# Kernel tuning notes

Measured on AMD Instinct MI355X. Metric: run time of the kernel, lower is better.

Reference implementation:

```python
import jax, jax.numpy as jnp
import numpy as np

N = 8192
INPUT_DIM = 512
R = 2
HID = INPUT_DIM // R  # 256
OUTPUT_DIM = 512


def _linear_params(key, out_dim, in_dim):
    kw, kb = jax.random.split(key)
    bound = 1.0 / np.sqrt(in_dim)
    w = jax.random.uniform(kw, (out_dim, in_dim), jnp.float32, -bound, bound)
    b = jax.random.uniform(kb, (out_dim,), jnp.float32, -bound, bound)
    return w, b


def setup_inputs() -> dict:
    key = jax.random.key(0)
    k0, k1, k2, k3, k4 = jax.random.split(key, 5)
    O0 = jax.random.normal(k0, (N, INPUT_DIM), dtype=jnp.float32)
    W_w, W_b = _linear_params(k1, HID, INPUT_DIM)
    U_w, U_b = _linear_params(k2, HID, INPUT_DIM)
    H_w, H_b = _linear_params(k3, HID, INPUT_DIM)
    fc0_w, fc0_b = _linear_params(k4, OUTPUT_DIM, HID)
    return {"O0": O0, "W_w": W_w, "W_b": W_b, "U_w": U_w, "U_b": U_b,
            "H_w": H_w, "H_b": H_b, "fc0_w": fc0_w, "fc0_b": fc0_b}


def reference(O0, W_w, W_b, U_w, U_b, H_w, H_b, fc0_w, fc0_b):
    q = O0 @ W_w.T + W_b          # [N, HID]
    k = O0 @ U_w.T + U_b          # [N, HID]
    v = O0 @ H_w.T + H_b          # [N, HID]
    # NOTE: no 1/sqrt(d) scaling, faithful to the original module.
    scores = q @ k.T              # [N, N]
    R1 = jax.nn.softmax(scores, axis=1)
    O1 = (R1 @ v) @ fc0_w.T + fc0_b  # [N, OUTPUT_DIM]
    return O1
```

## Files before the change

kernel.cpp:

```cpp
#include <hip/hip_runtime.h>

#define N_TOK 8192
#define IN_DIM 512
#define HID 256
#define OUT_DIM 512

typedef _Float16 v8h __attribute__((ext_vector_type(8)));
typedef float v4f __attribute__((ext_vector_type(4)));

__device__ inline void async_copy16(const void* g, void* l) {
    __builtin_amdgcn_global_load_lds(
        (const __attribute__((address_space(1))) void*)g,
        (__attribute__((address_space(3))) void*)l, 16, 0, 0);
}

__global__ __launch_bounds__(256)
void conv_f16(const float* __restrict__ in, _Float16* __restrict__ out) {
    const size_t i = ((size_t)blockIdx.x * 256 + threadIdx.x) * 8;
    float4 f0 = *(const float4*)&in[i];
    float4 f1 = *(const float4*)&in[i + 4];
    union { _Float16 h[8]; uint4 u; } pk;
    pk.h[0] = (_Float16)f0.x; pk.h[1] = (_Float16)f0.y;
    pk.h[2] = (_Float16)f0.z; pk.h[3] = (_Float16)f0.w;
    pk.h[4] = (_Float16)f1.x; pk.h[5] = (_Float16)f1.y;
    pk.h[6] = (_Float16)f1.z; pk.h[7] = (_Float16)f1.w;
    *(uint4*)&out[i] = pk.u;
}

__global__ __launch_bounds__(256)
void proj_qkv(const _Float16* __restrict__ O0h,
              const float* __restrict__ W_w, const float* __restrict__ W_b,
              const float* __restrict__ U_w, const float* __restrict__ U_b,
              const float* __restrict__ H_w, const float* __restrict__ H_b,
              _Float16* __restrict__ qb, _Float16* __restrict__ kb,
              _Float16* __restrict__ vt) {
    __shared__ _Float16 As[128][72];
    __shared__ _Float16 Bs[64][72];

    const int t = threadIdx.x;
    const int wv = t >> 6;
    const int lane = t & 63;
    const int quad = lane >> 4;
    const int lm = lane & 15;
    const int m0 = blockIdx.x * 128;
    const int n0 = blockIdx.y * 64;
    const int z = blockIdx.z;

    const float* B    = (z == 0) ? W_w : (z == 1) ? U_w : H_w;
    const float* bias = (z == 0) ? W_b : (z == 1) ? U_b : H_b;

    v4f acc[2][4];
#pragma unroll
    for (int rs = 0; rs < 2; rs++)
#pragma unroll
        for (int ct = 0; ct < 4; ct++) acc[rs][ct] = (v4f){0.f, 0.f, 0.f, 0.f};

    for (int k0 = 0; k0 < IN_DIM; k0 += 64) {
        __syncthreads();
#pragma unroll
        for (int i = 0; i < 4; i++) {
            int slot = t + 256 * i;
            int ar = slot >> 3, ac8 = slot & 7;
            *(uint4*)&As[ar][ac8 * 8] =
                *(const uint4*)&O0h[(size_t)(m0 + ar) * IN_DIM + k0 + ac8 * 8];
        }
#pragma unroll
        for (int i = 0; i < 4; i++) {
            int slot = t + 256 * i;
            int br = slot >> 4, bc4 = slot & 15;
            float4 f = *(const float4*)&B[(size_t)(n0 + br) * IN_DIM + k0 + bc4 * 4];
            union { _Float16 h[4]; uint2 u; } pk;
            pk.h[0] = (_Float16)f.x; pk.h[1] = (_Float16)f.y;
            pk.h[2] = (_Float16)f.z; pk.h[3] = (_Float16)f.w;
            *(uint2*)&Bs[br][bc4 * 4] = pk.u;
        }
        __syncthreads();

#pragma unroll
        for (int kc = 0; kc < 2; kc++) {
            v8h a0 = *(const v8h*)&As[wv * 32 + lm][kc * 32 + quad * 8];
            v8h a1 = *(const v8h*)&As[wv * 32 + 16 + lm][kc * 32 + quad * 8];
            v8h b[4];
#pragma unroll
            for (int ct = 0; ct < 4; ct++)
                b[ct] = *(const v8h*)&Bs[ct * 16 + lm][kc * 32 + quad * 8];
#pragma unroll
            for (int ct = 0; ct < 4; ct++) {
                acc[0][ct] = __builtin_amdgcn_mfma_f32_16x16x32_f16(a0, b[ct], acc[0][ct], 0, 0, 0);
                acc[1][ct] = __builtin_amdgcn_mfma_f32_16x16x32_f16(a1, b[ct], acc[1][ct], 0, 0, 0);
            }
        }
    }

    if (z < 2) {
        _Float16* outp = (z == 0) ? qb : kb;
#pragma unroll
        for (int rs = 0; rs < 2; rs++)
#pragma unroll
            for (int ct = 0; ct < 4; ct++) {
                const int col = n0 + ct * 16 + lm;
                const float bv = bias[col];
#pragma unroll
                for (int r = 0; r < 4; r++) {
                    const int row = m0 + wv * 32 + rs * 16 + quad * 4 + r;
                    outp[(size_t)row * HID + col] = (_Float16)(acc[rs][ct][r] + bv);
                }
            }
    } else {
#pragma unroll
        for (int rs = 0; rs < 2; rs++)
#pragma unroll
            for (int ct = 0; ct < 4; ct++) {
                const int col = n0 + ct * 16 + lm;
                const float bv = bias[col];
                const int rowbase = m0 + wv * 32 + rs * 16 + quad * 4;
                union { _Float16 h[4]; uint2 u; } pk;
#pragma unroll
                for (int r = 0; r < 4; r++) pk.h[r] = (_Float16)(acc[rs][ct][r] + bv);
                *(uint2*)&vt[(size_t)col * N_TOK + rowbase] = pk.u;
            }
    }
}

__global__ __launch_bounds__(256, 2)
void flash_mfma(const _Float16* __restrict__ qb, const _Float16* __restrict__ kb,
                const _Float16* __restrict__ vt,
                _Float16* __restrict__ partA,
                _Float16* __restrict__ partB,
                float* __restrict__ mbuf, float* __restrict__ lbuf,
                int keys_per_part) {
    __shared__ _Float16 Ks[32][256];
    __shared__ _Float16 Vs[2][256][32];

    const int t = threadIdx.x;
    const int w = t >> 6;
    const int lane = t & 63;
    const int quad = lane >> 4;
    const int lm = lane & 15;
    const int p = blockIdx.x & 7;
    const int m0 = (blockIdx.x >> 3) * 128 + w * 32;

    _Float16* part = (p < 4) ? partA + (size_t)p * N_TOK * HID
                             : partB + (size_t)(p - 4) * N_TOK * HID;

    v8h aq[2][8];
#pragma unroll
    for (int rs = 0; rs < 2; rs++)
#pragma unroll
        for (int c = 0; c < 8; c++)
            aq[rs][c] = *(const v8h*)&qb[(size_t)(m0 + rs * 16 + lm) * HID + c * 32 + quad * 8];

    v4f o[2][16];
    float mr[2], lr[2];
#pragma unroll
    for (int rs = 0; rs < 2; rs++) {
#pragma unroll
        for (int dt = 0; dt < 16; dt++) o[rs][dt] = (v4f){0.f, 0.f, 0.f, 0.f};
        mr[rs] = -1e30f; lr[rs] = 0.f;
    }

    const int n_start = p * keys_per_part;
    const int iters = keys_per_part / 32;

    auto issue_K = [&](int n0) {
#pragma unroll
        for (int i = 0; i < 4; i++) {
            int slot = t + 256 * i;
            int kr = slot >> 5, cpos = slot & 31;
            int kc = (cpos - kr) & 31;
            int m = kr & 15;
            int src = ((m >> 2) << 3) + ((kr >> 4) << 2) + (m & 3);
            async_copy16(&kb[(size_t)(n0 + src) * HID + kc * 8],
                         (_Float16*)Ks + (size_t)slot * 8);
        }
    };
    auto issue_V = [&](int n0, int b) {
#pragma unroll
        for (int i = 0; i < 4; i++) {
            int slot = t + 256 * i;
            int d = slot >> 2, c = slot & 3;
            async_copy16(&vt[(size_t)d * N_TOK + n0 + c * 8],
                         (_Float16*)Vs[b] + (size_t)slot * 8);
        }
    };

    issue_V(n_start, 0);
    issue_K(n_start);

    for (int it = 0; it < iters; it++) {
        __syncthreads();

        v4f s[2][2];
#pragma unroll
        for (int rs = 0; rs < 2; rs++)
#pragma unroll
            for (int nt = 0; nt < 2; nt++) s[rs][nt] = (v4f){0.f, 0.f, 0.f, 0.f};
#pragma unroll
        for (int c = 0; c < 8; c++) {
            const int kc = c * 4 + quad;
            const int cp0 = (kc + lm) & 31;
            const int cp1 = (kc + 16 + lm) & 31;
            v8h b0 = *(const v8h*)((const _Float16*)Ks + lm * 256 + cp0 * 8);
            v8h b1 = *(const v8h*)((const _Float16*)Ks + (16 + lm) * 256 + cp1 * 8);
            s[0][0] = __builtin_amdgcn_mfma_f32_16x16x32_f16(b0, aq[0][c], s[0][0], 0, 0, 0);
            s[0][1] = __builtin_amdgcn_mfma_f32_16x16x32_f16(b1, aq[0][c], s[0][1], 0, 0, 0);
            s[1][0] = __builtin_amdgcn_mfma_f32_16x16x32_f16(b0, aq[1][c], s[1][0], 0, 0, 0);
            s[1][1] = __builtin_amdgcn_mfma_f32_16x16x32_f16(b1, aq[1][c], s[1][1], 0, 0, 0);
        }

        __syncthreads();
        if (it + 1 < iters) {
            issue_K(n_start + (it + 1) * 32);
            issue_V(n_start + (it + 1) * 32, (it + 1) & 1);
        }

        v8h bp[2];
#pragma unroll
        for (int rs = 0; rs < 2; rs++) {
            float tm = s[rs][0][0];
#pragma unroll
            for (int r = 1; r < 4; r++) tm = fmaxf(tm, s[rs][0][r]);
#pragma unroll
            for (int r = 0; r < 4; r++) tm = fmaxf(tm, s[rs][1][r]);
            tm = fmaxf(tm, __shfl_xor(tm, 16));
            tm = fmaxf(tm, __shfl_xor(tm, 32));
            float mn = fmaxf(mr[rs], tm);
            if (__any((int)(mn > mr[rs]))) {
                float al = __expf(mr[rs] - mn);
                lr[rs] *= al;
#pragma unroll
                for (int dt = 0; dt < 16; dt++)
#pragma unroll
                    for (int r = 0; r < 4; r++) o[rs][dt][r] *= al;
            }
            mr[rs] = mn;
            float ls = 0.f;
            v8h bpv;
#pragma unroll
            for (int j = 0; j < 4; j++) {
                float p0 = __expf(s[rs][0][j] - mn);
                float p1 = __expf(s[rs][1][j] - mn);
                bpv[j] = (_Float16)p0;
                bpv[j + 4] = (_Float16)p1;
                ls += p0 + p1;
            }
            ls += __shfl_xor(ls, 16);
            ls += __shfl_xor(ls, 32);
            lr[rs] += ls;
            bp[rs] = bpv;
        }

        const _Float16* VsB = (const _Float16*)Vs[it & 1];
#pragma unroll
        for (int dt = 0; dt < 16; dt++) {
            v8h av = *(const v8h*)(VsB + (dt * 16 + lm) * 32 + quad * 8);
            o[0][dt] = __builtin_amdgcn_mfma_f32_16x16x32_f16(av, bp[0], o[0][dt], 0, 0, 0);
            o[1][dt] = __builtin_amdgcn_mfma_f32_16x16x32_f16(av, bp[1], o[1][dt], 0, 0, 0);
        }
    }

#pragma unroll
    for (int rs = 0; rs < 2; rs++) {
        const float inv = 1.0f / lr[rs];
        const int row = m0 + rs * 16 + lm;
#pragma unroll
        for (int dt = 0; dt < 16; dt++) {
            union { _Float16 h[4]; uint2 u; } pk;
#pragma unroll
            for (int r = 0; r < 4; r++) pk.h[r] = (_Float16)(o[rs][dt][r] * inv);
            *(uint2*)&part[(size_t)row * HID + dt * 16 + quad * 4] = pk.u;
        }
        if (quad == 0) {
            mbuf[p * N_TOK + row] = mr[rs];
            lbuf[p * N_TOK + row] = lr[rs];
        }
    }
}

__global__ __launch_bounds__(256)
void combine_parts(_Float16* __restrict__ attn,
                   const _Float16* __restrict__ partA, const _Float16* __restrict__ partB,
                   const float* __restrict__ mbuf, const float* __restrict__ lbuf,
                   int P) {
    const int gid = blockIdx.x * 256 + threadIdx.x;
    const int row = gid >> 5;
    const int c8 = (gid & 31) * 8;

    float M = -1e30f;
    for (int p = 0; p < P; p++) M = fmaxf(M, mbuf[p * N_TOK + row]);
    float den = 0.f;
    float acc[8];
#pragma unroll
    for (int j = 0; j < 8; j++) acc[j] = 0.f;
    for (int p = 0; p < P; p++) {
        float wgt = lbuf[p * N_TOK + row] * __expf(mbuf[p * N_TOK + row] - M);
        den += wgt;
        const _Float16* base = (p < 4) ? partA + (size_t)p * N_TOK * HID
                                       : partB + (size_t)(p - 4) * N_TOK * HID;
        v8h y = *(const v8h*)&base[(size_t)row * HID + c8];
#pragma unroll
        for (int j = 0; j < 8; j++) acc[j] += wgt * (float)y[j];
    }
    const float inv = 1.0f / den;
    union { _Float16 h[8]; uint4 u; } pk;
#pragma unroll
    for (int j = 0; j < 8; j++) pk.h[j] = (_Float16)(acc[j] * inv);
    *(uint4*)&attn[(size_t)row * HID + c8] = pk.u;
}

__global__ __launch_bounds__(256)
void mfma_fc0(const _Float16* __restrict__ Ah, const float* __restrict__ B,
              const float* __restrict__ bias, float* __restrict__ Cout,
              int K, int NC) {
    __shared__ _Float16 As[128][72];
    __shared__ _Float16 Bs[64][72];

    const int t = threadIdx.x;
    const int wv = t >> 6;
    const int lane = t & 63;
    const int quad = lane >> 4;
    const int lm = lane & 15;
    const int m0 = blockIdx.x * 128;
    const int n0 = blockIdx.y * 64;

    v4f acc[2][4];
#pragma unroll
    for (int rs = 0; rs < 2; rs++)
#pragma unroll
        for (int ct = 0; ct < 4; ct++) acc[rs][ct] = (v4f){0.f, 0.f, 0.f, 0.f};

    for (int k0 = 0; k0 < K; k0 += 64) {
        __syncthreads();
#pragma unroll
        for (int i = 0; i < 4; i++) {
            int slot = t + 256 * i;
            int ar = slot >> 3, ac8 = slot & 7;
            *(uint4*)&As[ar][ac8 * 8] =
                *(const uint4*)&Ah[(size_t)(m0 + ar) * K + k0 + ac8 * 8];
        }
#pragma unroll
        for (int i = 0; i < 4; i++) {
            int slot = t + 256 * i;
            int br = slot >> 4, bc4 = slot & 15;
            float4 f = *(const float4*)&B[(size_t)(n0 + br) * K + k0 + bc4 * 4];
            union { _Float16 h[4]; uint2 u; } pk;
            pk.h[0] = (_Float16)f.x; pk.h[1] = (_Float16)f.y;
            pk.h[2] = (_Float16)f.z; pk.h[3] = (_Float16)f.w;
            *(uint2*)&Bs[br][bc4 * 4] = pk.u;
        }
        __syncthreads();

#pragma unroll
        for (int kc = 0; kc < 2; kc++) {
            v8h a0 = *(const v8h*)&As[wv * 32 + lm][kc * 32 + quad * 8];
            v8h a1 = *(const v8h*)&As[wv * 32 + 16 + lm][kc * 32 + quad * 8];
            v8h b[4];
#pragma unroll
            for (int ct = 0; ct < 4; ct++)
                b[ct] = *(const v8h*)&Bs[ct * 16 + lm][kc * 32 + quad * 8];
#pragma unroll
            for (int ct = 0; ct < 4; ct++) {
                acc[0][ct] = __builtin_amdgcn_mfma_f32_16x16x32_f16(a0, b[ct], acc[0][ct], 0, 0, 0);
                acc[1][ct] = __builtin_amdgcn_mfma_f32_16x16x32_f16(a1, b[ct], acc[1][ct], 0, 0, 0);
            }
        }
    }

#pragma unroll
    for (int rs = 0; rs < 2; rs++)
#pragma unroll
        for (int ct = 0; ct < 4; ct++) {
            const int col = n0 + ct * 16 + lm;
            const float bv = bias[col];
#pragma unroll
            for (int r = 0; r < 4; r++) {
                const int row = m0 + wv * 32 + rs * 16 + quad * 4 + r;
                Cout[(size_t)row * NC + col] = acc[rs][ct][r] + bv;
            }
        }
}

extern "C" void kernel_launch(void* const* d_in, const int* in_sizes, int n_in,
                              void* d_out, int out_size, void* d_ws, size_t ws_size,
                              hipStream_t stream) {
    const float* O0    = (const float*)d_in[0];
    const float* W_w   = (const float*)d_in[1];
    const float* W_b   = (const float*)d_in[2];
    const float* U_w   = (const float*)d_in[3];
    const float* U_b   = (const float*)d_in[4];
    const float* H_w   = (const float*)d_in[5];
    const float* H_b   = (const float*)d_in[6];
    const float* fc0_w = (const float*)d_in[7];
    const float* fc0_b = (const float*)d_in[8];

    char* ws = (char*)d_ws;
    _Float16* qb    = (_Float16*)ws;
    _Float16* kb    = (_Float16*)(ws + ((size_t)4 << 20));
    _Float16* vt    = (_Float16*)(ws + ((size_t)8 << 20));
    float*    mbuf  = (float*)(ws + ((size_t)12 << 20));
    float*    lbuf  = mbuf + 8 * N_TOK;
    _Float16* partB = (_Float16*)(ws + ((size_t)16 << 20));
    _Float16* attn  = qb;
    _Float16* O0h   = (_Float16*)d_out;
    _Float16* partA = (_Float16*)d_out;

    const int P = 8;
    const int kpp = N_TOK / P;

    dim3 blk(256);
    conv_f16<<<dim3(N_TOK * IN_DIM / 8 / 256), blk, 0, stream>>>(O0, O0h);

    proj_qkv<<<dim3(N_TOK / 128, HID / 64, 3), blk, 0, stream>>>(
        O0h, W_w, W_b, U_w, U_b, H_w, H_b, qb, kb, vt);

    flash_mfma<<<dim3((N_TOK / 128) * P), blk, 0, stream>>>(
        qb, kb, vt, partA, partB, mbuf, lbuf, kpp);

    combine_parts<<<dim3(N_TOK * HID / 8 / 256), blk, 0, stream>>>(
        attn, partA, partB, mbuf, lbuf, P);

    mfma_fc0<<<dim3(N_TOK / 128, OUT_DIM / 64), blk, 0, stream>>>(
        attn, fc0_w, fc0_b, (float*)d_out, HID, OUT_DIM);
}
```

Baseline: 218.3 us.

## Pre-convert weights, double-buffer GEMM loads, use 512-thread flash blocks

All weight matrices are converted to fp16 in one combined conversion kernel with O0, so the projection and fc0 GEMMs no longer convert fp32 weights inside their tile loops. Those GEMMs now use async global-to-LDS copies into a double-buffered, XOR-swizzled shared layout that overlaps the next tile's load with MFMA work. The flash attention kernel moves to 512 threads, each wave owning 16 query rows instead of 32, to cut register pressure and raise occupancy. In exchange, each K/V tile is reused by fewer MFMAs per wave.

After: 234.7 us. 7.5% more time.

```diff
diff --git a/kernel.cpp b/kernel.cpp
--- a/kernel.cpp
+++ b/kernel.cpp
@@ -15,27 +15,42 @@
 }
 
 __global__ __launch_bounds__(256)
-void conv_f16(const float* __restrict__ in, _Float16* __restrict__ out) {
-    const size_t i = ((size_t)blockIdx.x * 256 + threadIdx.x) * 8;
-    float4 f0 = *(const float4*)&in[i];
-    float4 f1 = *(const float4*)&in[i + 4];
+void conv_all(const float* __restrict__ O0, const float* __restrict__ W_w,
+              const float* __restrict__ U_w, const float* __restrict__ H_w,
+              const float* __restrict__ fc0_w,
+              _Float16* __restrict__ O0h, _Float16* __restrict__ Wh,
+              _Float16* __restrict__ Uh, _Float16* __restrict__ Hh,
+              _Float16* __restrict__ fh) {
+    const int b = blockIdx.x;
+    const float* src; _Float16* dst; size_t off;
+    if (b < 2048) { src = O0; dst = O0h; off = (size_t)b * 2048; }
+    else {
+        int wsel = (b - 2048) >> 6, wb = (b - 2048) & 63;
+        src = (wsel == 0) ? W_w : (wsel == 1) ? U_w : (wsel == 2) ? H_w : fc0_w;
+        dst = (wsel == 0) ? Wh  : (wsel == 1) ? Uh  : (wsel == 2) ? Hh  : fh;
+        off = (size_t)wb * 2048;
+    }
+    const size_t i = off + (size_t)threadIdx.x * 8;
+    float4 f0 = *(const float4*)&src[i];
+    float4 f1 = *(const float4*)&src[i + 4];
     union { _Float16 h[8]; uint4 u; } pk;
     pk.h[0] = (_Float16)f0.x; pk.h[1] = (_Float16)f0.y;
     pk.h[2] = (_Float16)f0.z; pk.h[3] = (_Float16)f0.w;
     pk.h[4] = (_Float16)f1.x; pk.h[5] = (_Float16)f1.y;
     pk.h[6] = (_Float16)f1.z; pk.h[7] = (_Float16)f1.w;
-    *(uint4*)&out[i] = pk.u;
+    *(uint4*)&dst[i] = pk.u;
 }
 
 __global__ __launch_bounds__(256)
 void proj_qkv(const _Float16* __restrict__ O0h,
-              const float* __restrict__ W_w, const float* __restrict__ W_b,
-              const float* __restrict__ U_w, const float* __restrict__ U_b,
-              const float* __restrict__ H_w, const float* __restrict__ H_b,
+              const _Float16* __restrict__ Wh, const _Float16* __restrict__ Uh,
+              const _Float16* __restrict__ Hh,
+              const float* __restrict__ W_b, const float* __restrict__ U_b,
+              const float* __restrict__ H_b,
               _Float16* __restrict__ qb, _Float16* __restrict__ kb,
               _Float16* __restrict__ vt) {
-    __shared__ _Float16 As[128][72];
-    __shared__ _Float16 Bs[64][72];
+    __shared__ _Float16 As[2][128 * 64];
+    __shared__ _Float16 Bs[2][64 * 64];
 
     const int t = threadIdx.x;
     const int wv = t >> 6;
@@ -46,44 +61,52 @@
     const int n0 = blockIdx.y * 64;
     const int z = blockIdx.z;
 
-    const float* B    = (z == 0) ? W_w : (z == 1) ? U_w : H_w;
-    const float* bias = (z == 0) ? W_b : (z == 1) ? U_b : H_b;
-
-    v4f acc[2][4];
-#pragma unroll
-    for (int rs = 0; rs < 2; rs++)
-#pragma unroll
-        for (int ct = 0; ct < 4; ct++) acc[rs][ct] = (v4f){0.f, 0.f, 0.f, 0.f};
-
-    for (int k0 = 0; k0 < IN_DIM; k0 += 64) {
-        __syncthreads();
+    const _Float16* Bw  = (z == 0) ? Wh : (z == 1) ? Uh : Hh;
+    const float*    bias = (z == 0) ? W_b : (z == 1) ? U_b : H_b;
+
+    auto issue = [&](int k0, int b) {
 #pragma unroll
         for (int i = 0; i < 4; i++) {
             int slot = t + 256 * i;
-            int ar = slot >> 3, ac8 = slot & 7;
-            *(uint4*)&As[ar][ac8 * 8] =
-                *(const uint4*)&O0h[(size_t)(m0 + ar) * IN_DIM + k0 + ac8 * 8];
-        }
-#pragma unroll
-        for (int i = 0; i < 4; i++) {
+            int r = slot >> 3, cpos = slot & 7;
+            int c = (cpos - r) & 7;
+            async_copy16(&O0h[(size_t)(m0 + r) * IN_DIM + k0 + c * 8],
+                         (_Float16*)As[b] + (size_t)slot * 8);
+        }
+#pragma unroll
+        for (int i = 0; i < 2; i++) {
             int slot = t + 256 * i;
-            int br = slot >> 4, bc4 = slot & 15;
-            float4 f = *(const float4*)&B[(size_t)(n0 + br) * IN_DIM + k0 + bc4 * 4];
-            union { _Float16 h[4]; uint2 u; } pk;
-            pk.h[0] = (_Float16)f.x; pk.h[1] = (_Float16)f.y;
-            pk.h[2] = (_Float16)f.z; pk.h[3] = (_Float16)f.w;
-            *(uint2*)&Bs[br][bc4 * 4] = pk.u;
-        }
+            int r = slot >> 3, cpos = slot & 7;
+            int c = (cpos - r) & 7;
+            async_copy16(&Bw[(size_t)(n0 + r) * IN_DIM + k0 + c * 8],
+                         (_Float16*)Bs[b] + (size_t)slot * 8);
+        }
+    };
+
+    v4f acc[2][4];
+#pragma unroll
+    for (int rs = 0; rs < 2; rs++)
+#pragma unroll
+        for (int ct = 0; ct < 4; ct++) acc[rs][ct] = (v4f){0.f, 0.f, 0.f, 0.f};
+
+    issue(0, 0);
+    for (int it = 0; it < IN_DIM / 64; it++) {
+        const int buf = it & 1;
         __syncthreads();
+        if (it + 1 < IN_DIM / 64) issue((it + 1) * 64, buf ^ 1);
 
 #pragma unroll
         for (int kc = 0; kc < 2; kc++) {
-            v8h a0 = *(const v8h*)&As[wv * 32 + lm][kc * 32 + quad * 8];
-            v8h a1 = *(const v8h*)&As[wv * 32 + 16 + lm][kc * 32 + quad * 8];
+            const int ch = kc * 4 + quad;
+            const int rA0 = wv * 32 + lm, rA1 = rA0 + 16;
+            v8h a0 = *(const v8h*)(As[buf] + rA0 * 64 + ((ch + rA0) & 7) * 8);
+            v8h a1 = *(const v8h*)(As[buf] + rA1 * 64 + ((ch + rA1) & 7) * 8);
             v8h b[4];
 #pragma unroll
-            for (int ct = 0; ct < 4; ct++)
-                b[ct] = *(const v8h*)&Bs[ct * 16 + lm][kc * 32 + quad * 8];
+            for (int ct = 0; ct < 4; ct++) {
+                const int rB = ct * 16 + lm;
+                b[ct] = *(const v8h*)(Bs[buf] + rB * 64 + ((ch + rB) & 7) * 8);
+            }
 #pragma unroll
             for (int ct = 0; ct < 4; ct++) {
                 acc[0][ct] = __builtin_amdgcn_mfma_f32_16x16x32_f16(a0, b[ct], acc[0][ct], 0, 0, 0);
@@ -122,15 +145,15 @@
     }
 }
 
-__global__ __launch_bounds__(256, 2)
+__global__ __launch_bounds__(512, 4)
 void flash_mfma(const _Float16* __restrict__ qb, const _Float16* __restrict__ kb,
                 const _Float16* __restrict__ vt,
                 _Float16* __restrict__ partA,
                 _Float16* __restrict__ partB,
                 float* __restrict__ mbuf, float* __restrict__ lbuf,
                 int keys_per_part) {
-    __shared__ _Float16 Ks[32][256];
-    __shared__ _Float16 Vs[2][256][32];
+    __shared__ _Float16 Ks[32 * 256];
+    __shared__ _Float16 Vs[2][256 * 32];
 
     const int t = threadIdx.x;
     const int w = t >> 6;
@@ -138,34 +161,28 @@
     const int quad = lane >> 4;
     const int lm = lane & 15;
     const int p = blockIdx.x & 7;
-    const int m0 = (blockIdx.x >> 3) * 128 + w * 32;
+    const int m0 = (blockIdx.x >> 3) * 128 + w * 16;
 
     _Float16* part = (p < 4) ? partA + (size_t)p * N_TOK * HID
                              : partB + (size_t)(p - 4) * N_TOK * HID;
 
-    v8h aq[2][8];
-#pragma unroll
-    for (int rs = 0; rs < 2; rs++)
-#pragma unroll
-        for (int c = 0; c < 8; c++)
-            aq[rs][c] = *(const v8h*)&qb[(size_t)(m0 + rs * 16 + lm) * HID + c * 32 + quad * 8];
-
-    v4f o[2][16];
-    float mr[2], lr[2];
-#pragma unroll
-    for (int rs = 0; rs < 2; rs++) {
-#pragma unroll
-        for (int dt = 0; dt < 16; dt++) o[rs][dt] = (v4f){0.f, 0.f, 0.f, 0.f};
-        mr[rs] = -1e30f; lr[rs] = 0.f;
-    }
+    v8h aq[8];
+#pragma unroll
+    for (int c = 0; c < 8; c++)
+        aq[c] = *(const v8h*)&qb[(size_t)(m0 + lm) * HID + c * 32 + quad * 8];
+
+    v4f o[16];
+    float mr = -1e30f, lr = 0.f;
+#pragma unroll
+    for (int dt = 0; dt < 16; dt++) o[dt] = (v4f){0.f, 0.f, 0.f, 0.f};
 
     const int n_start = p * keys_per_part;
     const int iters = keys_per_part / 32;
 
     auto issue_K = [&](int n0) {
 #pragma unroll
-        for (int i = 0; i < 4; i++) {
-            int slot = t + 256 * i;
+        for (int i = 0; i < 2; i++) {
+            int slot = t + 512 * i;
             int kr = slot >> 5, cpos = slot & 31;
             int kc = (cpos - kr) & 31;
             int m = kr & 15;
@@ -176,8 +193,8 @@
     };
     auto issue_V = [&](int n0, int b) {
 #pragma unroll
-        for (int i = 0; i < 4; i++) {
-            int slot = t + 256 * i;
+        for (int i = 0; i < 2; i++) {
+            int slot = t + 512 * i;
             int d = slot >> 2, c = slot & 3;
             async_copy16(&vt[(size_t)d * N_TOK + n0 + c * 8],
                          (_Float16*)Vs[b] + (size_t)slot * 8);
@@ -190,22 +207,16 @@
     for (int it = 0; it < iters; it++) {
         __syncthreads();
 
-        v4f s[2][2];
-#pragma unroll
-        for (int rs = 0; rs < 2; rs++)
-#pragma unroll
-            for (int nt = 0; nt < 2; nt++) s[rs][nt] = (v4f){0.f, 0.f, 0.f, 0.f};
+        v4f s[2];
+        s[0] = (v4f){0.f, 0.f, 0.f, 0.f};
+        s[1] = (v4f){0.f, 0.f, 0.f, 0.f};
 #pragma unroll
         for (int c = 0; c < 8; c++) {
             const int kc = c * 4 + quad;
-            const int cp0 = (kc + lm) & 31;
-            const int cp1 = (kc + 16 + lm) & 31;
-            v8h b0 = *(const v8h*)((const _Float16*)Ks + lm * 256 + cp0 * 8);
-            v8h b1 = *(const v8h*)((const _Float16*)Ks + (16 + lm) * 256 + cp1 * 8);
-            s[0][0] = __builtin_amdgcn_mfma_f32_16x16x32_f16(b0, aq[0][c], s[0][0], 0, 0, 0);
-            s[0][1] = __builtin_amdgcn_mfma_f32_16x16x32_f16(b1, aq[0][c], s[0][1], 0, 0, 0);
-            s[1][0] = __builtin_amdgcn_mfma_f32_16x16x32_f16(b0, aq[1][c], s[1][0], 0, 0, 0);
-            s[1][1] = __builtin_amdgcn_mfma_f32_16x16x32_f16(b1, aq[1][c], s[1][1], 0, 0, 0);
+            v8h b0 = *(const v8h*)((const _Float16*)Ks + lm * 256 + ((kc + lm) & 31) * 8);
+            v8h b1 = *(const v8h*)((const _Float16*)Ks + (16 + lm) * 256 + ((kc + 16 + lm) & 31) * 8);
+            s[0] = __builtin_amdgcn_mfma_f32_16x16x32_f16(b0, aq[c], s[0], 0, 0, 0);
+            s[1] = __builtin_amdgcn_mfma_f32_16x16x32_f16(b1, aq[c], s[1], 0, 0, 0);
         }
 
         __syncthreads();
@@ -214,66 +225,57 @@
             issue_V(n_start + (it + 1) * 32, (it + 1) & 1);
         }
 
-        v8h bp[2];
-#pragma unroll
-        for (int rs = 0; rs < 2; rs++) {
-            float tm = s[rs][0][0];
-#pragma unroll
-            for (int r = 1; r < 4; r++) tm = fmaxf(tm, s[rs][0][r]);
-#pragma unroll
-            for (int r = 0; r < 4; r++) tm = fmaxf(tm, s[rs][1][r]);
-            tm = fmaxf(tm, __shfl_xor(tm, 16));
-            tm = fmaxf(tm, __shfl_xor(tm, 32));
-            float mn = fmaxf(mr[rs], tm);
-            if (__any((int)(mn > mr[rs]))) {
-                float al = __expf(mr[rs] - mn);
-                lr[rs] *= al;
-#pragma unroll
-                for (int dt = 0; dt < 16; dt++)
-#pragma unroll
-                    for (int r = 0; r < 4; r++) o[rs][dt][r] *= al;
-            }
-            mr[rs] = mn;
-            float ls = 0.f;
-            v8h bpv;
-#pragma unroll
-            for (int j = 0; j < 4; j++) {
-                float p0 = __expf(s[rs][0][j] - mn);
-                float p1 = __expf(s[rs][1][j] - mn);
-                bpv[j] = (_Float16)p0;
-                bpv[j + 4] = (_Float16)p1;
-                ls += p0 + p1;
-            }
-            ls += __shfl_xor(ls, 16);
-            ls += __shfl_xor(ls, 32);
-            lr[rs] += ls;
-            bp[rs] = bpv;
-        }
+        float tm = s[0][0];
+#pragma unroll
+        for (int r = 1; r < 4; r++) tm = fmaxf(tm, s[0][r]);
+#pragma unroll
+        for (int r = 0; r < 4; r++) tm = fmaxf(tm, s[1][r]);
+        tm = fmaxf(tm, __shfl_xor(tm, 16));
+        tm = fmaxf(tm, __shfl_xor(tm, 32));
+        float mn = fmaxf(mr, tm);
+        if (__any((int)(mn > mr))) {
+            float al = __expf(mr - mn);
+            lr *= al;
+#pragma unroll
+            for (int dt = 0; dt < 16; dt++)
+#pragma unroll
+                for (int r = 0; r < 4; r++) o[dt][r] *= al;
+        }
+        mr = mn;
+        float ls = 0.f;
+        v8h bp;
+#pragma unroll
+        for (int j = 0; j < 4; j++) {
+            float p0 = __expf(s[0][j] - mn);
+            float p1 = __expf(s[1][j] - mn);
+            bp[j] = (_Float16)p0;
+            bp[j + 4] = (_Float16)p1;
+            ls += p0 + p1;
+        }
+        ls += __shfl_xor(ls, 16);
+        ls += __shfl_xor(ls, 32);
+        lr += ls;
 
         const _Float16* VsB = (const _Float16*)Vs[it & 1];
 #pragma unroll
         for (int dt = 0; dt < 16; dt++) {
             v8h av = *(const v8h*)(VsB + (dt * 16 + lm) * 32 + quad * 8);
-            o[0][dt] = __builtin_amdgcn_mfma_f32_16x16x32_f16(av, bp[0], o[0][dt], 0, 0, 0);
-            o[1][dt] = __builtin_amdgcn_mfma_f32_16x16x32_f16(av, bp[1], o[1][dt], 0, 0, 0);
-        }
-    }
-
-#pragma unroll
-    for (int rs = 0; rs < 2; rs++) {
-        const float inv = 1.0f / lr[rs];
-        const int row = m0 + rs * 16 + lm;
-#pragma unroll
-        for (int dt = 0; dt < 16; dt++) {
-            union { _Float16 h[4]; uint2 u; } pk;
-#pragma unroll
-            for (int r = 0; r < 4; r++) pk.h[r] = (_Float16)(o[rs][dt][r] * inv);
-            *(uint2*)&part[(size_t)row * HID + dt * 16 + quad * 4] = pk.u;
-        }
-        if (quad == 0) {
-            mbuf[p * N_TOK + row] = mr[rs];
-            lbuf[p * N_TOK + row] = lr[rs];
-        }
+            o[dt] = __builtin_amdgcn_mfma_f32_16x16x32_f16(av, bp, o[dt], 0, 0, 0);
+        }
+    }
+
+    const float inv = 1.0f / lr;
+    const int row = m0 + lm;
+#pragma unroll
+    for (int dt = 0; dt < 16; dt++) {
+        union { _Float16 h[4]; uint2 u; } pk;
+#pragma unroll
+        for (int r = 0; r < 4; r++) pk.h[r] = (_Float16)(o[dt][r] * inv);
+        *(uint2*)&part[(size_t)row * HID + dt * 16 + quad * 4] = pk.u;
+    }
+    if (quad == 0) {
+        mbuf[p * N_TOK + row] = mr;
+        lbuf[p * N_TOK + row] = lr;
     }
 }
 
@@ -309,11 +311,10 @@
 }
 
 __global__ __launch_bounds__(256)
-void mfma_fc0(const _Float16* __restrict__ Ah, const float* __restrict__ B,
-              const float* __restrict__ bias, float* __restrict__ Cout,
-              int K, int NC) {
-    __shared__ _Float16 As[128][72];
-    __shared__ _Float16 Bs[64][72];
+void mfma_fc0(const _Float16* __restrict__ Ah, const _Float16* __restrict__ Bh,
+              const float* __restrict__ bias, float* __restrict__ Cout) {
+    __shared__ _Float16 As[2][128 * 64];
+    __shared__ _Float16 Bs[2][64 * 64];
 
     const int t = threadIdx.x;
     const int wv = t >> 6;
@@ -323,41 +324,49 @@
     const int m0 = blockIdx.x * 128;
     const int n0 = blockIdx.y * 64;
 
-    v4f acc[2][4];
-#pragma unroll
-    for (int rs = 0; rs < 2; rs++)
-#pragma unroll
-        for (int ct = 0; ct < 4; ct++) acc[rs][ct] = (v4f){0.f, 0.f, 0.f, 0.f};
-
-    for (int k0 = 0; k0 < K; k0 += 64) {
-        __syncthreads();
+    auto issue = [&](int k0, int b) {
 #pragma unroll
         for (int i = 0; i < 4; i++) {
             int slot = t + 256 * i;
-            int ar = slot >> 3, ac8 = slot & 7;
-            *(uint4*)&As[ar][ac8 * 8] =
-                *(const uint4*)&Ah[(size_t)(m0 + ar) * K + k0 + ac8 * 8];
-        }
-#pragma unroll
-        for (int i = 0; i < 4; i++) {
+            int r = slot >> 3, cpos = slot & 7;
+            int c = (cpos - r) & 7;
+            async_copy16(&Ah[(size_t)(m0 + r) * HID + k0 + c * 8],
+                         (_Float16*)As[b] + (size_t)slot * 8);
+        }
+#pragma unroll
+        for (int i = 0; i < 2; i++) {
             int slot = t + 256 * i;
-            int br = slot >> 4, bc4 = slot & 15;
-            float4 f = *(const float4*)&B[(size_t)(n0 + br) * K + k0 + bc4 * 4];
-            union { _Float16 h[4]; uint2 u; } pk;
-            pk.h[0] = (_Float16)f.x; pk.h[1] = (_Float16)f.y;
-            pk.h[2] = (_Float16)f.z; pk.h[3] = (_Float16)f.w;
-            *(uint2*)&Bs[br][bc4 * 4] = pk.u;
-        }
+            int r = slot >> 3, cpos = slot & 7;
+            int c = (cpos - r) & 7;
+            async_copy16(&Bh[(size_t)(n0 + r) * HID + k0 + c * 8],
+                         (_Float16*)Bs[b] + (size_t)slot * 8);
+        }
+    };
+
+    v4f acc[2][4];
+#pragma unroll
+    for (int rs = 0; rs < 2; rs++)
+#pragma unroll
+        for (int ct = 0; ct < 4; ct++) acc[rs][ct] = (v4f){0.f, 0.f, 0.f, 0.f};
+
+    issue(0, 0);
+    for (int it = 0; it < HID / 64; it++) {
+        const int buf = it & 1;
         __syncthreads();
+        if (it + 1 < HID / 64) issue((it + 1) * 64, buf ^ 1);
 
 #pragma unroll
         for (int kc = 0; kc < 2; kc++) {
-            v8h a0 = *(const v8h*)&As[wv * 32 + lm][kc * 32 + quad * 8];
-            v8h a1 = *(const v8h*)&As[wv * 32 + 16 + lm][kc * 32 + quad * 8];
+            const int ch = kc * 4 + quad;
+            const int rA0 = wv * 32 + lm, rA1 = rA0 + 16;
+            v8h a0 = *(const v8h*)(As[buf] + rA0 * 64 + ((ch + rA0) & 7) * 8);
+            v8h a1 = *(const v8h*)(As[buf] + rA1 * 64 + ((ch + rA1) & 7) * 8);
             v8h b[4];
 #pragma unroll
-            for (int ct = 0; ct < 4; ct++)
-                b[ct] = *(const v8h*)&Bs[ct * 16 + lm][kc * 32 + quad * 8];
+            for (int ct = 0; ct < 4; ct++) {
+                const int rB = ct * 16 + lm;
+                b[ct] = *(const v8h*)(Bs[buf] + rB * 64 + ((ch + rB) & 7) * 8);
+            }
 #pragma unroll
             for (int ct = 0; ct < 4; ct++) {
                 acc[0][ct] = __builtin_amdgcn_mfma_f32_16x16x32_f16(a0, b[ct], acc[0][ct], 0, 0, 0);
@@ -375,7 +384,7 @@
 #pragma unroll
             for (int r = 0; r < 4; r++) {
                 const int row = m0 + wv * 32 + rs * 16 + quad * 4 + r;
-                Cout[(size_t)row * NC + col] = acc[rs][ct][r] + bv;
+                Cout[(size_t)row * OUT_DIM + col] = acc[rs][ct][r] + bv;
             }
         }
 }
@@ -399,6 +408,10 @@
     _Float16* vt    = (_Float16*)(ws + ((size_t)8 << 20));
     float*    mbuf  = (float*)(ws + ((size_t)12 << 20));
     float*    lbuf  = mbuf + 8 * N_TOK;
+    _Float16* Wh    = (_Float16*)(ws + ((size_t)12 << 20) + ((size_t)512 << 10));
+    _Float16* Uh    = Wh + (size_t)HID * IN_DIM;
+    _Float16* Hh    = Uh + (size_t)HID * IN_DIM;
+    _Float16* fh    = Hh + (size_t)HID * IN_DIM;
     _Float16* partB = (_Float16*)(ws + ((size_t)16 << 20));
     _Float16* attn  = qb;
     _Float16* O0h   = (_Float16*)d_out;
@@ -407,18 +420,18 @@
     const int P = 8;
     const int kpp = N_TOK / P;
 
-    dim3 blk(256);
-    conv_f16<<<dim3(N_TOK * IN_DIM / 8 / 256), blk, 0, stream>>>(O0, O0h);
-
-    proj_qkv<<<dim3(N_TOK / 128, HID / 64, 3), blk, 0, stream>>>(
-        O0h, W_w, W_b, U_w, U_b, H_w, H_b, qb, kb, vt);
-
-    flash_mfma<<<dim3((N_TOK / 128) * P), blk, 0, stream>>>(
+    conv_all<<<dim3(2048 + 256), dim3(256), 0, stream>>>(
+        O0, W_w, U_w, H_w, fc0_w, O0h, Wh, Uh, Hh, fh);
+
+    proj_qkv<<<dim3(N_TOK / 128, HID / 64, 3), dim3(256), 0, stream>>>(
+        O0h, Wh, Uh, Hh, W_b, U_b, H_b, qb, kb, vt);
+
+    flash_mfma<<<dim3((N_TOK / 128) * P), dim3(512), 0, stream>>>(
         qb, kb, vt, partA, partB, mbuf, lbuf, kpp);
 
-    combine_parts<<<dim3(N_TOK * HID / 8 / 256), blk, 0, stream>>>(
+    combine_parts<<<dim3(N_TOK * HID / 8 / 256), dim3(256), 0, stream>>>(
         attn, partA, partB, mbuf, lbuf, P);
 
-    mfma_fc0<<<dim3(N_TOK / 128, OUT_DIM / 64), blk, 0, stream>>>(
-        attn, fc0_w, fc0_b, (float*)d_out, HID, OUT_DIM);
-}
+    mfma_fc0<<<dim3(N_TOK / 128, OUT_DIM / 64), dim3(256), 0, stream>>>(
+        attn, fh, fc0_b, (float*)d_out);
+}
```
